# Performance work log

Hardware: AMD Instinct MI355X
Metric: run time of the kernel (lower is better)

## Reference

```python
import jax, jax.numpy as jnp
import numpy as np

USER_NUM = 100000
POI_NUM = 120
EMB = 64
HID1, HID2 = 256, 128
HEADS, ATT_H = 6, 8
SEQ = 5
CI_VOCAB = 50000
N_EDGES_U = 1600000


def _gcn_conv(x, edge_index, W, b, n):
    # PyG GCNConv: add self loops, symmetric D^-1/2 (A+I) D^-1/2 normalization
    x = x @ W
    loops = jnp.arange(n)
    src = jnp.concatenate([edge_index[0], loops])
    dst = jnp.concatenate([edge_index[1], loops])
    deg = jax.ops.segment_sum(jnp.ones_like(dst, x.dtype), dst, num_segments=n)
    dinv = jnp.where(deg > 0, jax.lax.rsqrt(deg), 0.0)
    norm = dinv[src] * dinv[dst]
    out = jax.ops.segment_sum(x[src] * norm[:, None], dst, num_segments=n)
    return out + b


def setup_inputs() -> dict:
    key = jax.random.key(0)
    ks = jax.random.split(key, 30)
    f = lambda k, shape, fan_in: (jax.random.normal(k, shape, jnp.float32) / np.sqrt(fan_in)).astype(jnp.float32)
    inp = {}
    inp['edge_user'] = jnp.stack([
        jax.random.randint(ks[0], (USER_NUM, SEQ), 0, USER_NUM),
        jax.random.randint(ks[1], (USER_NUM, SEQ), 0, CI_VOCAB)])
    inp['edge_poi'] = jax.random.randint(ks[2], (2, 4000), 0, POI_NUM)
    inp['u_v_edge'] = jax.random.randint(ks[3], (2, N_EDGES_U), 0, USER_NUM)
    inp['v_u_edge'] = jax.random.randint(ks[4], (2, 4000), 0, POI_NUM)
    inp['user_table'] = f(ks[5], (USER_NUM, EMB), EMB)
    inp['ci_table'] = f(ks[6], (CI_VOCAB, EMB), EMB)
    inp['ci_table2'] = f(ks[7], (CI_VOCAB, EMB), EMB)
    inp['gcn1_w'] = f(ks[8], (EMB, EMB), EMB)
    inp['gcn1_b'] = jnp.zeros((EMB,), jnp.float32)
    inp['gcn2_w'] = f(ks[9], (EMB, EMB), EMB)
    inp['gcn2_b'] = jnp.zeros((EMB,), jnp.float32)
    inp['at_w'] = f(ks[10], (HEADS, EMB, ATT_H), EMB)
    inp['at_b'] = jnp.zeros((HEADS, ATT_H), jnp.float32)
    inp['d2_w'] = f(ks[11], (1 + HEADS * ATT_H, 1), 1 + HEADS * ATT_H)  # Linear(49,1)
    inp['d2_b'] = jnp.zeros((1,), jnp.float32)
    inp['d1u_w'] = f(ks[12], (EMB, HID1), EMB)
    inp['d1u_b'] = jnp.zeros((HID1,), jnp.float32)
    inp['d2u_w'] = f(ks[13], (HID1, HID2), HID1)
    inp['d2u_b'] = jnp.zeros((HID2,), jnp.float32)
    inp['d3u_w'] = f(ks[14], (HID2, POI_NUM), HID2)
    inp['d3u_b'] = jnp.zeros((POI_NUM,), jnp.float32)
    inp['d1_w'] = f(ks[15], (EMB, POI_NUM), EMB)  # dense1_: Linear(n_emb, 120)
    inp['d1_b'] = jnp.zeros((POI_NUM,), jnp.float32)
    return inp


def reference(edge_user, edge_poi, u_v_edge, v_u_edge, user_table, ci_table, ci_table2,
              gcn1_w, gcn1_b, gcn2_w, gcn2_b, at_w, at_b, d2_w, d2_b,
              d1u_w, d1u_b, d2u_w, d2u_b, d3u_w, d3u_b, d1_w, d1_b):
    # user GCN stack (dropout treated as identity / eval mode)
    ue = _gcn_conv(user_table, u_v_edge, gcn1_w, gcn1_b, USER_NUM)
    ue = jax.nn.relu(ue)
    ue = _gcn_conv(ue, u_v_edge, gcn2_w, gcn2_b, USER_NUM)  # (U, EMB)

    ci_ids = edge_user[1]            # (U, SEQ) check-in ids
    ci = ci_table[ci_ids]            # (U, SEQ, EMB)
    ci2 = ci_table2[ci_ids]          # (U, SEQ, EMB)

    # batched multi-head tiny attention: softmax over the SEQ axis per user
    w = jnp.einsum('usd,hdk->uhsk', ci, at_w) + at_b[None, :, None, :]
    beta = jax.nn.softmax(jnp.tanh(w), axis=2)                       # (U, H, SEQ, ATT_H)
    beta = jnp.transpose(beta, (0, 2, 1, 3)).reshape(ci.shape[0], SEQ, HEADS * ATT_H)
    att = jnp.transpose(beta, (0, 2, 1))                              # (U, 48, SEQ)
    use_trans = att @ ci                                              # (U, 48, EMB)

    uef = jnp.concatenate([ue[:, None, :], use_trans], axis=1)       # (U, 49, EMB)
    uef = jnp.transpose(uef, (0, 2, 1)) @ d2_w + d2_b                # (U, EMB, 1)
    uef = uef[..., 0]                                                # (U, EMB)

    h = jax.nn.relu(uef @ d1u_w + d1u_b)
    h = jax.nn.relu(h @ d2u_w + d2u_b)
    score1 = h @ d3u_w + d3u_b                                       # (U, POI_NUM)

    score2 = jnp.sum(ci2 @ d1_w + d1_b, axis=1)                      # (U, POI_NUM)
    return score1 + score2
```

## Files before the change

### kernel.cpp

```cpp
#include <hip/hip_runtime.h>

#define U_NUM 100000
#define NE    1600000
#define SEQL  5

#define OFF_DEG      0UL
#define OFF_CURSOR   400000UL
#define OFF_ROWSTART 800000UL
#define OFF_DINV     1200016UL
#define OFF_BSUM     1600016UL
#define OFF_CSR      1600528UL
#define OFF_XS       8000528UL
#define OFF_B        20800528UL
#define OFF_CI2B     46400528UL
#define OFF_CIB      52800528UL

#define NB    196
#define BSH   9
#define BCAP  12240
#define OFF_BINS  OFF_XS
#define OFF_GCUR  (OFF_BINS + (size_t)NB * BCAP * 8)

typedef __attribute__((ext_vector_type(8))) short bf16x8;
typedef __attribute__((ext_vector_type(4))) float f32x4;

__device__ __forceinline__ float rd_lane(float v, int l) {
    return __int_as_float(__builtin_amdgcn_readlane(__float_as_int(v), l));
}

__device__ __forceinline__ short f2bf(float f) {
    unsigned u = __float_as_uint(f);
    unsigned r = (u + 0x7fffu + ((u >> 16) & 1u)) >> 16;
    return (short)r;
}

__device__ __forceinline__ unsigned pk2(float a, float b) {
    return ((unsigned)(unsigned short)f2bf(a)) | (((unsigned)(unsigned short)f2bf(b)) << 16);
}

__device__ __forceinline__ float bflo(unsigned p) { return __uint_as_float(p << 16); }
__device__ __forceinline__ float bfhi(unsigned p) { return __uint_as_float(p & 0xffff0000u); }

__device__ __forceinline__ int swzo(int row, int bytecol, int rowstride) {
    return row * rowstride + (bytecol ^ ((row & 7) << 4));
}

__global__ __launch_bounds__(256) void k_count(const int* __restrict__ edge, int* __restrict__ deg) {
    int e = blockIdx.x * 256 + threadIdx.x;
    atomicAdd(&deg[edge[NE + e]], 1);
}

__global__ __launch_bounds__(256) void k_dinv(const int* __restrict__ deg, float* __restrict__ dinv) {
    int i = blockIdx.x * 256 + threadIdx.x;
    if (i < U_NUM) dinv[i] = rsqrtf((float)(deg[i] + 1));
}

__global__ __launch_bounds__(256) void k_cvt2(const float* __restrict__ src, unsigned* __restrict__ dst) {
    int i = blockIdx.x * 256 + threadIdx.x;
    float2 v = *(const float2*)(src + (size_t)i * 2);
    dst[i] = pk2(v.x, v.y);
}

__global__ __launch_bounds__(1024) void k_scanA(const int* __restrict__ deg, int* __restrict__ bsum) {
    __shared__ int sm[1024];
    int i = blockIdx.x * 1024 + threadIdx.x;
    sm[threadIdx.x] = (i < U_NUM) ? deg[i] : 0;
    __syncthreads();
    for (int off = 512; off > 0; off >>= 1) {
        if (threadIdx.x < off) sm[threadIdx.x] += sm[threadIdx.x + off];
        __syncthreads();
    }
    if (threadIdx.x == 0) bsum[blockIdx.x] = sm[0];
}

__global__ void k_scanB(int* bsum, int nb) {
    if (threadIdx.x == 0) {
        int acc = 0;
        for (int b = 0; b < nb; ++b) { int v = bsum[b]; bsum[b] = acc; acc += v; }
    }
}

__global__ __launch_bounds__(1024) void k_scanC(const int* __restrict__ deg, const int* __restrict__ bsum,
                                                int* __restrict__ row_start) {
    __shared__ int sm[1024];
    int t = threadIdx.x;
    int i = blockIdx.x * 1024 + t;
    int v = (i < U_NUM) ? deg[i] : 0;
    sm[t] = v;
    __syncthreads();
    for (int off = 1; off < 1024; off <<= 1) {
        int x = (t >= off) ? sm[t - off] : 0;
        __syncthreads();
        sm[t] += x;
        __syncthreads();
    }
    int incl = sm[t];
    int base = bsum[blockIdx.x];
    if (i < U_NUM) row_start[i] = base + incl - v;
    if (i == U_NUM - 1) row_start[U_NUM] = base + incl;
}

__global__ __launch_bounds__(256) void k_binA(const int* __restrict__ edge,
                                              unsigned* __restrict__ gcur,
                                              uint2* __restrict__ bins) {
    __shared__ int hist[256];
    __shared__ int startx[256];
    __shared__ int cur[256];
    __shared__ int gbase[256];
    __shared__ uint2 stage[4096];
    int t = threadIdx.x;
    int base = blockIdx.x * 4096;
    hist[t] = 0; cur[t] = 0;
    __syncthreads();
    int src[16], dst[16];
#pragma unroll
    for (int j = 0; j < 16; ++j) {
        int e = base + j * 256 + t;
        src[j] = 0; dst[j] = -1;
        if (e < NE) {
            src[j] = edge[e];
            dst[j] = edge[NE + e];
            atomicAdd(&hist[dst[j] >> BSH], 1);
        }
    }
    __syncthreads();
    startx[t] = hist[t];
    __syncthreads();
    for (int off = 1; off < 256; off <<= 1) {
        int v = (t >= off) ? startx[t - off] : 0;
        __syncthreads();
        startx[t] += v;
        __syncthreads();
    }
    {
        int ex = startx[t] - hist[t];
        __syncthreads();
        startx[t] = ex;
    }
    if (t < NB) gbase[t] = (int)atomicAdd(&gcur[t], (unsigned)hist[t]);
    __syncthreads();
#pragma unroll
    for (int j = 0; j < 16; ++j) {
        if (dst[j] >= 0) {
            int b = dst[j] >> BSH;
            int p = startx[b] + atomicAdd(&cur[b], 1);
            stage[p] = make_uint2((unsigned)src[j], (unsigned)dst[j]);
        }
    }
    __syncthreads();
    int cnt = NE - base; if (cnt > 4096) cnt = 4096;
    for (int p = t; p < cnt; p += 256) {
        uint2 v = stage[p];
        int b = (int)(v.y >> BSH);
        bins[(size_t)b * BCAP + gbase[b] + (p - startx[b])] = v;
    }
}

__global__ __launch_bounds__(256) void k_fillB(const uint2* __restrict__ bins,
                                               const unsigned* __restrict__ gcur,
                                               const int* __restrict__ row_start,
                                               int* __restrict__ csr) {
    __shared__ int cur[512];
    int b = blockIdx.x, t = threadIdx.x;
    cur[t] = 0; cur[t + 256] = 0;
    __syncthreads();
    int cnt = (int)gcur[b];
    int d0 = b << BSH;
    for (int i = t; i < cnt; i += 256) {
        uint2 e = bins[(size_t)b * BCAP + i];
        int d = (int)e.y;
        int pos = row_start[d] + atomicAdd(&cur[d - d0], 1);
        csr[pos] = (int)e.x;
    }
}

__global__ __launch_bounds__(256) void k_gemm64_mfma(
        const float* __restrict__ x, const float* __restrict__ w,
        const float* __restrict__ dinv, unsigned* __restrict__ outb, int relu_in) {
    __shared__ __align__(16) short Xa[64 * 64];
    __shared__ float dv[64];
    int t = threadIdx.x;
    int lane = t & 63, wid = t >> 6;
    int l15 = lane & 15, lg = lane >> 4;
    bf16x8 wf[2];
#pragma unroll
    for (int ks = 0; ks < 2; ++ks) {
        int col = wid * 16 + l15;
        int kb = ks * 32 + lg * 8;
        bf16x8 f;
#pragma unroll
        for (int j = 0; j < 8; ++j) f[j] = f2bf(w[(kb + j) * 64 + col]);
        wf[ks] = f;
    }
    int u0 = blockIdx.x * 64;
    {
        int ur = t >> 2, d0 = (t & 3) * 16;
        int u = u0 + ur;
        float xv[16];
        if (u < U_NUM) {
            const float4* up = (const float4*)(x + (size_t)u * 64 + d0);
#pragma unroll
            for (int q = 0; q < 4; ++q) {
                float4 v = up[q];
                xv[q * 4 + 0] = v.x; xv[q * 4 + 1] = v.y; xv[q * 4 + 2] = v.z; xv[q * 4 + 3] = v.w;
            }
        } else {
#pragma unroll
            for (int q = 0; q < 16; ++q) xv[q] = 0.f;
        }
        if (relu_in) {
#pragma unroll
            for (int q = 0; q < 16; ++q) xv[q] = fmaxf(xv[q], 0.f);
        }
        bf16x8 p0, p1;
#pragma unroll
        for (int j = 0; j < 8; ++j) { p0[j] = f2bf(xv[j]); p1[j] = f2bf(xv[8 + j]); }
        *(bf16x8*)((char*)Xa + swzo(ur, d0 * 2, 128)) = p0;
        *(bf16x8*)((char*)Xa + swzo(ur, d0 * 2 + 16, 128)) = p1;
        if (t < 64) {
            int uu = u0 + t;
            dv[t] = dinv[(uu < U_NUM) ? uu : (U_NUM - 1)];
        }
    }
    __syncthreads();
#pragma unroll
    for (int mt = 0; mt < 4; ++mt) {
        bf16x8 a0 = *(bf16x8*)((char*)Xa + swzo(mt * 16 + l15, lg * 16, 128));
        bf16x8 a1 = *(bf16x8*)((char*)Xa + swzo(mt * 16 + l15, 64 + lg * 16, 128));
        f32x4 c = {0.f, 0.f, 0.f, 0.f};
        c = __builtin_amdgcn_mfma_f32_16x16x32_bf16(a0, wf[0], c, 0, 0, 0);
        c = __builtin_amdgcn_mfma_f32_16x16x32_bf16(a1, wf[1], c, 0, 0, 0);
        int col = wid * 16 + l15;
#pragma unroll
        for (int r = 0; r < 4; ++r) {
            int row = mt * 16 + lg * 4 + r;
            float v = c[r] * dv[row];
            float other = __shfl_xor(v, 1);
            int u = u0 + row;
            if (!(l15 & 1) && u < U_NUM)
                outb[(size_t)u * 32 + (col >> 1)] = pk2(v, other);
        }
    }
}

__global__ __launch_bounds__(256) void k_gather2(const unsigned* __restrict__ xs, const float* __restrict__ dinv,
                                                 const int* __restrict__ row_start, const int* __restrict__ csr,
                                                 const float* __restrict__ bias, float* __restrict__ outb) {
    int i = blockIdx.x * 4 + (threadIdx.x >> 6);
    int lane = threadIdx.x & 63, half = lane >> 5, sl = lane & 31;
    int s0 = row_start[i], s1 = row_start[i + 1];
    float di = dinv[i];
    float accx = 0.f, accy = 0.f;
    if (!half) {
        unsigned pk = xs[(size_t)i * 32 + sl];
        accx = bflo(pk); accy = bfhi(pk);
    }
    int e = s0 + half;
    for (; e + 14 < s1; e += 16) {
        int id0 = csr[e], id1 = csr[e + 2], id2 = csr[e + 4], id3 = csr[e + 6];
        int id4 = csr[e + 8], id5 = csr[e + 10], id6 = csr[e + 12], id7 = csr[e + 14];
        unsigned p0 = xs[(size_t)id0 * 32 + sl];
        unsigned p1 = xs[(size_t)id1 * 32 + sl];
        unsigned p2 = xs[(size_t)id2 * 32 + sl];
        unsigned p3 = xs[(size_t)id3 * 32 + sl];
        unsigned p4 = xs[(size_t)id4 * 32 + sl];
        unsigned p5 = xs[(size_t)id5 * 32 + sl];
        unsigned p6 = xs[(size_t)id6 * 32 + sl];
        unsigned p7 = xs[(size_t)id7 * 32 + sl];
        accx += ((bflo(p0) + bflo(p1)) + (bflo(p2) + bflo(p3))) +
                ((bflo(p4) + bflo(p5)) + (bflo(p6) + bflo(p7)));
        accy += ((bfhi(p0) + bfhi(p1)) + (bfhi(p2) + bfhi(p3))) +
                ((bfhi(p4) + bfhi(p5)) + (bfhi(p6) + bfhi(p7)));
    }
    for (; e < s1; e += 2) {
        unsigned pa = xs[(size_t)csr[e] * 32 + sl];
        accx += bflo(pa);
        accy += bfhi(pa);
    }
    accx += __shfl_xor(accx, 32);
    accy += __shfl_xor(accy, 32);
    if (!half) {
        float2 bb = *(const float2*)(bias + sl * 2);
        float2 o;
        o.x = fmaf(accx, di, bb.x);
        o.y = fmaf(accy, di, bb.y);
        *(float2*)(outb + (size_t)i * 64 + sl * 2) = o;
    }
}

#define AUB 32

__global__ __launch_bounds__(256) void k_attn_mfma(
        const int* __restrict__ edge_user, const unsigned* __restrict__ cib,
        const unsigned* __restrict__ ci2b,
        const float* __restrict__ at_w, const float* __restrict__ at_b,
        const float* __restrict__ d2_w, const float* __restrict__ d2_b,
        const float* ue, unsigned* uefc) {
    __shared__ __align__(16) short CI[256 * 64];
    int t = threadIdx.x;
    int lane = t & 63, wid = t >> 6;
    int l15 = lane & 15, lg = lane >> 4;
    int half = lane >> 5, sl = lane & 31;

    bf16x8 bw[3][2];
#pragma unroll
    for (int nt = 0; nt < 3; ++nt) {
        int j48 = nt * 16 + l15;
        int h = j48 >> 3, kk = j48 & 7;
#pragma unroll
        for (int ks = 0; ks < 2; ++ks) {
            int kb = ks * 32 + lg * 8;
            bf16x8 f;
#pragma unroll
            for (int j = 0; j < 8; ++j) f[j] = f2bf(at_w[h * 512 + (kb + j) * 8 + kk]);
            bw[nt][ks] = f;
        }
    }
    float atbv[3], dcoef[3];
#pragma unroll
    for (int nt = 0; nt < 3; ++nt) {
        atbv[nt] = at_b[nt * 16 + l15];
        dcoef[nt] = d2_w[1 + nt * 16 + l15];
    }
    float d2w0 = d2_w[0], d2b0 = d2_b[0];

    int u0 = blockIdx.x * AUB;
    float accx[8], accy[8];
#pragma unroll
    for (int j = 0; j < 8; ++j) { accx[j] = 0.f; accy[j] = 0.f; }
#pragma unroll
    for (int j = 0; j < 8; ++j) {
#pragma unroll
        for (int q = 0; q < 4; ++q) {
            int s = q * 2 + half;
            int row = wid * 64 + j * 8 + s;
            unsigned pk = 0;
            if (s < 5) {
                int id = edge_user[U_NUM * SEQL + (u0 + wid * 8 + j) * SEQL + s];
                pk = cib[(size_t)id * 32 + sl];
                unsigned pc = ci2b[(size_t)id * 32 + sl];
                accx[j] += bflo(pc);
                accy[j] += bfhi(pc);
            }
            *(unsigned*)((char*)CI + swzo(row, sl * 4, 128)) = pk;
        }
    }
    __syncthreads();

    float evenm = (lg & 1) ? 0.f : 1.f;
    for (int mt = 0; mt < 4; ++mt) {
        int tbase = (wid * 4 + mt) * 16;
        bf16x8 a0 = *(bf16x8*)((char*)CI + swzo(tbase + l15, lg * 16, 128));
        bf16x8 a1 = *(bf16x8*)((char*)CI + swzo(tbase + l15, 64 + lg * 16, 128));
        float g0 = 0.f, g1 = 0.f, g2 = 0.f, g3 = 0.f;
#pragma unroll
        for (int nt = 0; nt < 3; ++nt) {
            f32x4 c = {0.f, 0.f, 0.f, 0.f};
            c = __builtin_amdgcn_mfma_f32_16x16x32_bf16(a0, bw[nt][0], c, 0, 0, 0);
            c = __builtin_amdgcn_mfma_f32_16x16x32_bf16(a1, bw[nt][1], c, 0, 0, 0);
            float w0 = c[0] + atbv[nt], w1 = c[1] + atbv[nt],
                  w2 = c[2] + atbv[nt], w3 = c[3] + atbv[nt];
            float e0 = __expf(1.f - __fdividef(2.f, __expf(2.f * w0) + 1.f));
            float e1 = __expf(1.f - __fdividef(2.f, __expf(2.f * w1) + 1.f));
            float e2 = __expf(1.f - __fdividef(2.f, __expf(2.f * w2) + 1.f));
            float e3 = __expf(1.f - __fdividef(2.f, __expf(2.f * w3) + 1.f));
            float partial = e0 + evenm * (e1 + e2 + e3);
            float esum = partial + __shfl_xor(partial, 16);
            float sc = __fdividef(dcoef[nt], esum);
            g0 = fmaf(e0, sc, g0);
            g1 = fmaf(e1, sc, g1);
            g2 = fmaf(e2, sc, g2);
            g3 = fmaf(e3, sc, g3);
        }
#pragma unroll
        for (int d = 1; d < 16; d <<= 1) {
            g0 += __shfl_xor(g0, d);
            g1 += __shfl_xor(g1, d);
            g2 += __shfl_xor(g2, d);
            g3 += __shfl_xor(g3, d);
        }
        float gA0 = rd_lane(g0, 0), gA1 = rd_lane(g1, 0), gA2 = rd_lane(g2, 0),
              gA3 = rd_lane(g3, 0), gA4 = rd_lane(g0, 16);
        float gB0 = rd_lane(g0, 32), gB1 = rd_lane(g1, 32), gB2 = rd_lane(g2, 32),
              gB3 = rd_lane(g3, 32), gB4 = rd_lane(g0, 48);
        float gs0 = half ? gB0 : gA0;
        float gs1 = half ? gB1 : gA1;
        float gs2 = half ? gB2 : gA2;
        float gs3 = half ? gB3 : gA3;
        float gs4 = half ? gB4 : gA4;
        int urow = tbase + half * 8;
        int u = u0 + (tbase >> 3) + half;
        float2 uev = *(const float2*)(ue + (size_t)u * 64 + sl * 2);
        float rx = fmaf(d2w0, uev.x, d2b0);
        float ry = fmaf(d2w0, uev.y, d2b0);
        unsigned c0 = *(unsigned*)((char*)CI + swzo(urow + 0, sl * 4, 128));
        unsigned c1 = *(unsigned*)((char*)CI + swzo(urow + 1, sl * 4, 128));
        unsigned c2 = *(unsigned*)((char*)CI + swzo(urow + 2, sl * 4, 128));
        unsigned c3 = *(unsigned*)((char*)CI + swzo(urow + 3, sl * 4, 128));
        unsigned c4 = *(unsigned*)((char*)CI + swzo(urow + 4, sl * 4, 128));
        rx = fmaf(gs0, bflo(c0), rx); ry = fmaf(gs0, bfhi(c0), ry);
        rx = fmaf(gs1, bflo(c1), rx); ry = fmaf(gs1, bfhi(c1), ry);
        rx = fmaf(gs2, bflo(c2), rx); ry = fmaf(gs2, bfhi(c2), ry);
        rx = fmaf(gs3, bflo(c3), rx); ry = fmaf(gs3, bfhi(c3), ry);
        rx = fmaf(gs4, bflo(c4), rx); ry = fmaf(gs4, bfhi(c4), ry);
        uefc[(size_t)u * 64 + sl] = pk2(rx, ry);
    }
#pragma unroll
    for (int j = 0; j < 8; ++j) {
        float ax = accx[j] + __shfl_xor(accx[j], 32);
        float ay = accy[j] + __shfl_xor(accy[j], 32);
        if (!half) {
            int u = u0 + wid * 8 + j;
            uefc[(size_t)u * 64 + 32 + sl] = pk2(ax, ay);
        }
    }
}

#define N_TILES 1563

__global__ __launch_bounds__(512, 4) void k_mlp_mfma(
        const unsigned* __restrict__ uefc,
        const float* __restrict__ w1, const float* __restrict__ b1,
        const float* __restrict__ w2, const float* __restrict__ b2,
        const float* __restrict__ w3, const float* __restrict__ b3,
        const float* __restrict__ dw, const float* __restrict__ db,
        float* __restrict__ out) {
    __shared__ __align__(16) short Xa[64 * 64];
    __shared__ __align__(16) short Ca[64 * 64];
    __shared__ __align__(16) short h1a[64 * 256];
    __shared__ __align__(16) short h2c[64 * 128];
    int t = threadIdx.x;
    int lane = t & 63, w = t >> 6;
    int l15 = lane & 15, lg = lane >> 4;

    bf16x8 wf1[4];
#pragma unroll
    for (int nt = 0; nt < 2; ++nt)
#pragma unroll
        for (int ks = 0; ks < 2; ++ks) {
            int col = w * 32 + nt * 16 + l15;
            int kb = ks * 32 + lg * 8;
            bf16x8 f;
#pragma unroll
            for (int j = 0; j < 8; ++j) f[j] = f2bf(w1[(kb + j) * 256 + col]);
            wf1[nt * 2 + ks] = f;
        }
    bf16x8 wf2[8];
#pragma unroll
    for (int ks = 0; ks < 8; ++ks) {
        int col = w * 16 + l15;
        int kb = ks * 32 + lg * 8;
        bf16x8 f;
#pragma unroll
        for (int j = 0; j < 8; ++j) f[j] = f2bf(w2[(kb + j) * 128 + col]);
        wf2[ks] = f;
    }
    bf16x8 wf3[6];
#pragma unroll
    for (int ks = 0; ks < 6; ++ks) {
        int col = w * 16 + l15;
        int kb = ks * 32 + lg * 8;
        bf16x8 f;
#pragma unroll
        for (int j = 0; j < 8; ++j) {
            int k = kb + j;
            float v = 0.f;
            if (col < 120) v = (k < 128) ? w3[k * 120 + col] : dw[(k - 128) * 120 + col];
            f[j] = f2bf(v);
        }
        wf3[ks] = f;
    }
    float bias1[2], bias2, bias3;
#pragma unroll
    for (int nt = 0; nt < 2; ++nt) bias1[nt] = b1[w * 32 + nt * 16 + l15];
    {
        int col = w * 16 + l15;
        bias2 = b2[col];
        bias3 = (col < 120) ? (b3[col] + 5.f * db[col]) : 0.f;
    }

    int ur = t >> 3, q = t & 7;
    for (int tile = blockIdx.x; tile < N_TILES; tile += gridDim.x) {
        int u0 = tile * 64;
        {
            size_t u = (size_t)u0 + ur;
            uint4 A0 = {0, 0, 0, 0}, A1 = A0;
            if (u < U_NUM) {
                const uint4* up = (const uint4*)(uefc + u * 64 + q * 8);
                A0 = up[0]; A1 = up[1];
            }
            char* base = (q < 4) ? ((char*)Xa) : ((char*)Ca);
            int bc = (q & 3) * 32;
            *(uint4*)(base + swzo(ur, bc, 128)) = A0;
            *(uint4*)(base + swzo(ur, bc + 16, 128)) = A1;
        }
        __syncthreads();
#pragma unroll
        for (int mt = 0; mt < 4; ++mt) {
            bf16x8 a0 = *(bf16x8*)((char*)Xa + swzo(mt * 16 + l15, lg * 16, 128));
            bf16x8 a1 = *(bf16x8*)((char*)Xa + swzo(mt * 16 + l15, 64 + lg * 16, 128));
#pragma unroll
            for (int nt = 0; nt < 2; ++nt) {
                f32x4 c = {0.f, 0.f, 0.f, 0.f};
                c = __builtin_amdgcn_mfma_f32_16x16x32_bf16(a0, wf1[nt * 2 + 0], c, 0, 0, 0);
                c = __builtin_amdgcn_mfma_f32_16x16x32_bf16(a1, wf1[nt * 2 + 1], c, 0, 0, 0);
                int col = w * 32 + nt * 16 + l15;
                float bb = bias1[nt];
#pragma unroll
                for (int r = 0; r < 4; ++r) {
                    int row = mt * 16 + lg * 4 + r;
                    *(short*)((char*)h1a + swzo(row, col * 2, 512)) = f2bf(fmaxf(c[r] + bb, 0.f));
                }
            }
        }
        __syncthreads();
#pragma unroll
        for (int mt = 0; mt < 4; ++mt) {
            bf16x8 af[8];
#pragma unroll
            for (int ks = 0; ks < 8; ++ks)
                af[ks] = *(bf16x8*)((char*)h1a + swzo(mt * 16 + l15, ks * 64 + lg * 16, 512));
            f32x4 c = {0.f, 0.f, 0.f, 0.f};
#pragma unroll
            for (int ks = 0; ks < 8; ++ks)
                c = __builtin_amdgcn_mfma_f32_16x16x32_bf16(af[ks], wf2[ks], c, 0, 0, 0);
            int col = w * 16 + l15;
#pragma unroll
            for (int r = 0; r < 4; ++r) {
                int row = mt * 16 + lg * 4 + r;
                *(short*)((char*)h2c + swzo(row, col * 2, 256)) = f2bf(fmaxf(c[r] + bias2, 0.f));
            }
        }
        __syncthreads();
        float* Obuf = (float*)h1a;
#pragma unroll
        for (int mt = 0; mt < 4; ++mt) {
            bf16x8 af[6];
#pragma unroll
            for (int ks = 0; ks < 4; ++ks)
                af[ks] = *(bf16x8*)((char*)h2c + swzo(mt * 16 + l15, ks * 64 + lg * 16, 256));
#pragma unroll
            for (int ks = 4; ks < 6; ++ks)
                af[ks] = *(bf16x8*)((char*)Ca + swzo(mt * 16 + l15, (ks - 4) * 64 + lg * 16, 128));
            f32x4 c = {0.f, 0.f, 0.f, 0.f};
#pragma unroll
            for (int ks = 0; ks < 6; ++ks)
                c = __builtin_amdgcn_mfma_f32_16x16x32_bf16(af[ks], wf3[ks], c, 0, 0, 0);
            int col = w * 16 + l15;
            if (col < 120) {
#pragma unroll
                for (int r = 0; r < 4; ++r)
                    Obuf[(mt * 16 + lg * 4 + r) * 124 + col] = c[r] + bias3;
            }
        }
        __syncthreads();
        {
            int nrow = (U_NUM - u0 < 64) ? (U_NUM - u0) : 64;
            int nfl4 = nrow * 30;
            for (int i = t; i < nfl4; i += 512) {
                int row = i / 30, ch = i - row * 30;
                float4 v = *(const float4*)(Obuf + row * 124 + ch * 4);
                *(float4*)(out + (size_t)(u0 + row) * 120 + ch * 4) = v;
            }
        }
        __syncthreads();
    }
}

extern "C" void kernel_launch(void* const* d_in, const int* in_sizes, int n_in,
                              void* d_out, int out_size, void* d_ws, size_t ws_size,
                              hipStream_t stream) {
    const int* edge_user   = (const int*)d_in[0];
    const int* u_v_edge    = (const int*)d_in[2];
    const float* user_table = (const float*)d_in[4];
    const float* ci_table   = (const float*)d_in[5];
    const float* ci_table2  = (const float*)d_in[6];
    const float* gcn1_w = (const float*)d_in[7];
    const float* gcn1_b = (const float*)d_in[8];
    const float* gcn2_w = (const float*)d_in[9];
    const float* gcn2_b = (const float*)d_in[10];
    const float* at_w = (const float*)d_in[11];
    const float* at_b = (const float*)d_in[12];
    const float* d2_w = (const float*)d_in[13];
    const float* d2_b = (const float*)d_in[14];
    const float* d1u_w = (const float*)d_in[15];
    const float* d1u_b = (const float*)d_in[16];
    const float* d2u_w = (const float*)d_in[17];
    const float* d2u_b = (const float*)d_in[18];
    const float* d3u_w = (const float*)d_in[19];
    const float* d3u_b = (const float*)d_in[20];
    const float* d1_w = (const float*)d_in[21];
    const float* d1_b = (const float*)d_in[22];
    float* out = (float*)d_out;
    char* ws = (char*)d_ws;

    int* deg       = (int*)(ws + OFF_DEG);
    int* row_start = (int*)(ws + OFF_ROWSTART);
    float* dinv    = (float*)(ws + OFF_DINV);
    int* bsum      = (int*)(ws + OFF_BSUM);
    int* csr       = (int*)(ws + OFF_CSR);
    unsigned* XS   = (unsigned*)(ws + OFF_XS);
    float* B       = (float*)(ws + OFF_B);
    unsigned* CI2B = (unsigned*)(ws + OFF_CI2B);
    unsigned* CIB  = (unsigned*)(ws + OFF_CIB);
    uint2* bins    = (uint2*)(ws + OFF_BINS);
    unsigned* gcur = (unsigned*)(ws + OFF_GCUR);

    hipMemsetAsync(ws, 0, 400000, stream);
    hipMemsetAsync(ws + OFF_GCUR, 0, NB * 4, stream);
    k_count<<<6250, 256, 0, stream>>>(u_v_edge, deg);
    k_cvt2<<<6250, 256, 0, stream>>>(ci_table, CIB);
    k_cvt2<<<6250, 256, 0, stream>>>(ci_table2, CI2B);
    k_dinv<<<391, 256, 0, stream>>>(deg, dinv);
    k_scanA<<<98, 1024, 0, stream>>>(deg, bsum);
    k_scanB<<<1, 64, 0, stream>>>(bsum, 98);
    k_scanC<<<98, 1024, 0, stream>>>(deg, bsum, row_start);
    k_binA<<<391, 256, 0, stream>>>(u_v_edge, gcur, bins);
    k_fillB<<<NB, 256, 0, stream>>>(bins, gcur, row_start, csr);

    k_gemm64_mfma<<<1563, 256, 0, stream>>>(user_table, gcn1_w, dinv, XS, 0);
    k_gather2<<<25000, 256, 0, stream>>>(XS, dinv, row_start, csr, gcn1_b, B);
    k_gemm64_mfma<<<1563, 256, 0, stream>>>(B, gcn2_w, dinv, XS, 1);
    k_gather2<<<25000, 256, 0, stream>>>(XS, dinv, row_start, csr, gcn2_b, B);

    k_attn_mfma<<<3125, 256, 0, stream>>>(edge_user, CIB, CI2B, at_w, at_b, d2_w, d2_b,
                                          B, (unsigned*)B);
    k_mlp_mfma<<<512, 512, 0, stream>>>((const unsigned*)B,
                                        d1u_w, d1u_b, d2u_w, d2u_b, d3u_w, d3u_b, d1_w, d1_b, out);
}
```

Measured before the change: 469.6 us.

## Fuse attention stage into persistent MLP kernel via shared-memory handoff

Merges the attention kernel into the persistent MLP kernel. Each 64-user tile now gathers check-in embeddings, runs the attention MFMAs and writes the per-user feature and ci2 sum straight into the shared-memory MLP input buffers, so the uefc intermediate no longer makes a round trip through global memory and one launch is removed. Attention weights are staged once per block in LDS and the h1 buffer is reused as gather scratch. Output stores become nontemporal. In exchange, the grid drops to 512 persistent blocks, so fewer waves are in flight to hide the random embedding gathers, and LDS use per block grows, which may lower occupancy.

```diff
diff --git a/kernel.cpp b/kernel.cpp
--- a/kernel.cpp
+++ b/kernel.cpp
@@ -5,7 +5,6 @@
 #define SEQL  5
 
 #define OFF_DEG      0UL
-#define OFF_CURSOR   400000UL
 #define OFF_ROWSTART 800000UL
 #define OFF_DINV     1200016UL
 #define OFF_BSUM     1600016UL
@@ -288,150 +287,27 @@
     }
 }
 
-#define AUB 32
-
-__global__ __launch_bounds__(256) void k_attn_mfma(
+#define N_TILES 1563
+
+__global__ __launch_bounds__(512, 4) void k_attn_mlp(
         const int* __restrict__ edge_user, const unsigned* __restrict__ cib,
-        const unsigned* __restrict__ ci2b,
+        const unsigned* __restrict__ ci2b, const float* __restrict__ ue,
         const float* __restrict__ at_w, const float* __restrict__ at_b,
         const float* __restrict__ d2_w, const float* __restrict__ d2_b,
-        const float* ue, unsigned* uefc) {
-    __shared__ __align__(16) short CI[256 * 64];
-    int t = threadIdx.x;
-    int lane = t & 63, wid = t >> 6;
-    int l15 = lane & 15, lg = lane >> 4;
-    int half = lane >> 5, sl = lane & 31;
-
-    bf16x8 bw[3][2];
-#pragma unroll
-    for (int nt = 0; nt < 3; ++nt) {
-        int j48 = nt * 16 + l15;
-        int h = j48 >> 3, kk = j48 & 7;
-#pragma unroll
-        for (int ks = 0; ks < 2; ++ks) {
-            int kb = ks * 32 + lg * 8;
-            bf16x8 f;
-#pragma unroll
-            for (int j = 0; j < 8; ++j) f[j] = f2bf(at_w[h * 512 + (kb + j) * 8 + kk]);
-            bw[nt][ks] = f;
-        }
-    }
-    float atbv[3], dcoef[3];
-#pragma unroll
-    for (int nt = 0; nt < 3; ++nt) {
-        atbv[nt] = at_b[nt * 16 + l15];
-        dcoef[nt] = d2_w[1 + nt * 16 + l15];
-    }
-    float d2w0 = d2_w[0], d2b0 = d2_b[0];
-
-    int u0 = blockIdx.x * AUB;
-    float accx[8], accy[8];
-#pragma unroll
-    for (int j = 0; j < 8; ++j) { accx[j] = 0.f; accy[j] = 0.f; }
-#pragma unroll
-    for (int j = 0; j < 8; ++j) {
-#pragma unroll
-        for (int q = 0; q < 4; ++q) {
-            int s = q * 2 + half;
-            int row = wid * 64 + j * 8 + s;
-            unsigned pk = 0;
-            if (s < 5) {
-                int id = edge_user[U_NUM * SEQL + (u0 + wid * 8 + j) * SEQL + s];
-                pk = cib[(size_t)id * 32 + sl];
-                unsigned pc = ci2b[(size_t)id * 32 + sl];
-                accx[j] += bflo(pc);
-                accy[j] += bfhi(pc);
-            }
-            *(unsigned*)((char*)CI + swzo(row, sl * 4, 128)) = pk;
-        }
-    }
-    __syncthreads();
-
-    float evenm = (lg & 1) ? 0.f : 1.f;
-    for (int mt = 0; mt < 4; ++mt) {
-        int tbase = (wid * 4 + mt) * 16;
-        bf16x8 a0 = *(bf16x8*)((char*)CI + swzo(tbase + l15, lg * 16, 128));
-        bf16x8 a1 = *(bf16x8*)((char*)CI + swzo(tbase + l15, 64 + lg * 16, 128));
-        float g0 = 0.f, g1 = 0.f, g2 = 0.f, g3 = 0.f;
-#pragma unroll
-        for (int nt = 0; nt < 3; ++nt) {
-            f32x4 c = {0.f, 0.f, 0.f, 0.f};
-            c = __builtin_amdgcn_mfma_f32_16x16x32_bf16(a0, bw[nt][0], c, 0, 0, 0);
-            c = __builtin_amdgcn_mfma_f32_16x16x32_bf16(a1, bw[nt][1], c, 0, 0, 0);
-            float w0 = c[0] + atbv[nt], w1 = c[1] + atbv[nt],
-                  w2 = c[2] + atbv[nt], w3 = c[3] + atbv[nt];
-            float e0 = __expf(1.f - __fdividef(2.f, __expf(2.f * w0) + 1.f));
-            float e1 = __expf(1.f - __fdividef(2.f, __expf(2.f * w1) + 1.f));
-            float e2 = __expf(1.f - __fdividef(2.f, __expf(2.f * w2) + 1.f));
-            float e3 = __expf(1.f - __fdividef(2.f, __expf(2.f * w3) + 1.f));
-            float partial = e0 + evenm * (e1 + e2 + e3);
-            float esum = partial + __shfl_xor(partial, 16);
-            float sc = __fdividef(dcoef[nt], esum);
-            g0 = fmaf(e0, sc, g0);
-            g1 = fmaf(e1, sc, g1);
-            g2 = fmaf(e2, sc, g2);
-            g3 = fmaf(e3, sc, g3);
-        }
-#pragma unroll
-        for (int d = 1; d < 16; d <<= 1) {
-            g0 += __shfl_xor(g0, d);
-            g1 += __shfl_xor(g1, d);
-            g2 += __shfl_xor(g2, d);
-            g3 += __shfl_xor(g3, d);
-        }
-        float gA0 = rd_lane(g0, 0), gA1 = rd_lane(g1, 0), gA2 = rd_lane(g2, 0),
-              gA3 = rd_lane(g3, 0), gA4 = rd_lane(g0, 16);
-        float gB0 = rd_lane(g0, 32), gB1 = rd_lane(g1, 32), gB2 = rd_lane(g2, 32),
-              gB3 = rd_lane(g3, 32), gB4 = rd_lane(g0, 48);
-        float gs0 = half ? gB0 : gA0;
-        float gs1 = half ? gB1 : gA1;
-        float gs2 = half ? gB2 : gA2;
-        float gs3 = half ? gB3 : gA3;
-        float gs4 = half ? gB4 : gA4;
-        int urow = tbase + half * 8;
-        int u = u0 + (tbase >> 3) + half;
-        float2 uev = *(const float2*)(ue + (size_t)u * 64 + sl * 2);
-        float rx = fmaf(d2w0, uev.x, d2b0);
-        float ry = fmaf(d2w0, uev.y, d2b0);
-        unsigned c0 = *(unsigned*)((char*)CI + swzo(urow + 0, sl * 4, 128));
-        unsigned c1 = *(unsigned*)((char*)CI + swzo(urow + 1, sl * 4, 128));
-        unsigned c2 = *(unsigned*)((char*)CI + swzo(urow + 2, sl * 4, 128));
-        unsigned c3 = *(unsigned*)((char*)CI + swzo(urow + 3, sl * 4, 128));
-        unsigned c4 = *(unsigned*)((char*)CI + swzo(urow + 4, sl * 4, 128));
-        rx = fmaf(gs0, bflo(c0), rx); ry = fmaf(gs0, bfhi(c0), ry);
-        rx = fmaf(gs1, bflo(c1), rx); ry = fmaf(gs1, bfhi(c1), ry);
-        rx = fmaf(gs2, bflo(c2), rx); ry = fmaf(gs2, bfhi(c2), ry);
-        rx = fmaf(gs3, bflo(c3), rx); ry = fmaf(gs3, bfhi(c3), ry);
-        rx = fmaf(gs4, bflo(c4), rx); ry = fmaf(gs4, bfhi(c4), ry);
-        uefc[(size_t)u * 64 + sl] = pk2(rx, ry);
-    }
-#pragma unroll
-    for (int j = 0; j < 8; ++j) {
-        float ax = accx[j] + __shfl_xor(accx[j], 32);
-        float ay = accy[j] + __shfl_xor(accy[j], 32);
-        if (!half) {
-            int u = u0 + wid * 8 + j;
-            uefc[(size_t)u * 64 + 32 + sl] = pk2(ax, ay);
-        }
-    }
-}
-
-#define N_TILES 1563
-
-__global__ __launch_bounds__(512, 4) void k_mlp_mfma(
-        const unsigned* __restrict__ uefc,
         const float* __restrict__ w1, const float* __restrict__ b1,
         const float* __restrict__ w2, const float* __restrict__ b2,
         const float* __restrict__ w3, const float* __restrict__ b3,
         const float* __restrict__ dw, const float* __restrict__ db,
         float* __restrict__ out) {
+    __shared__ __align__(16) short hbuf[64 * 256];
     __shared__ __align__(16) short Xa[64 * 64];
     __shared__ __align__(16) short Ca[64 * 64];
-    __shared__ __align__(16) short h1a[64 * 256];
     __shared__ __align__(16) short h2c[64 * 128];
+    __shared__ __align__(16) short BWL[6 * 64 * 8];
     int t = threadIdx.x;
     int lane = t & 63, w = t >> 6;
     int l15 = lane & 15, lg = lane >> 4;
+    int half = lane >> 5, sl = lane & 31;
 
     bf16x8 wf1[4];
 #pragma unroll
@@ -478,21 +354,123 @@
         bias2 = b2[col];
         bias3 = (col < 120) ? (b3[col] + 5.f * db[col]) : 0.f;
     }
-
-    int ur = t >> 3, q = t & 7;
+    float atbv[3], dcoef[3];
+#pragma unroll
+    for (int nt = 0; nt < 3; ++nt) {
+        atbv[nt] = at_b[nt * 16 + l15];
+        dcoef[nt] = d2_w[1 + nt * 16 + l15];
+    }
+    float d2w0 = d2_w[0], d2b0 = d2_b[0];
+    if (t < 64) {
+#pragma unroll
+        for (int nt = 0; nt < 3; ++nt) {
+            int j48 = nt * 16 + l15;
+            int hh = j48 >> 3, kk = j48 & 7;
+#pragma unroll
+            for (int ks = 0; ks < 2; ++ks) {
+                int kb = ks * 32 + lg * 8;
+                bf16x8 f;
+#pragma unroll
+                for (int j = 0; j < 8; ++j) f[j] = f2bf(at_w[hh * 512 + (kb + j) * 8 + kk]);
+                *(bf16x8*)(BWL + ((nt * 2 + ks) * 64 + lane) * 8) = f;
+            }
+        }
+    }
+    __syncthreads();
+
+    float evenm = (lg & 1) ? 0.f : 1.f;
     for (int tile = blockIdx.x; tile < N_TILES; tile += gridDim.x) {
         int u0 = tile * 64;
-        {
-            size_t u = (size_t)u0 + ur;
-            uint4 A0 = {0, 0, 0, 0}, A1 = A0;
-            if (u < U_NUM) {
-                const uint4* up = (const uint4*)(uefc + u * 64 + q * 8);
-                A0 = up[0]; A1 = up[1];
-            }
-            char* base = (q < 4) ? ((char*)Xa) : ((char*)Ca);
-            int bc = (q & 3) * 32;
-            *(uint4*)(base + swzo(ur, bc, 128)) = A0;
-            *(uint4*)(base + swzo(ur, bc + 16, 128)) = A1;
+#pragma unroll
+        for (int hh = 0; hh < 2; ++hh) {
+            float accx[4] = {0.f, 0.f, 0.f, 0.f}, accy[4] = {0.f, 0.f, 0.f, 0.f};
+#pragma unroll
+            for (int j = 0; j < 4; ++j) {
+#pragma unroll
+                for (int q = 0; q < 4; ++q) {
+                    int s = q * 2 + half;
+                    int row = w * 32 + j * 8 + s;
+                    int uu = u0 + 32 * hh + w * 4 + j;
+                    unsigned pk = 0;
+                    if (s < 5 && uu < U_NUM) {
+                        int id = edge_user[U_NUM * SEQL + uu * SEQL + s];
+                        pk = cib[(size_t)id * 32 + sl];
+                        unsigned pc = ci2b[(size_t)id * 32 + sl];
+                        accx[j] += bflo(pc);
+                        accy[j] += bfhi(pc);
+                    }
+                    *(unsigned*)((char*)hbuf + swzo(row, sl * 4, 128)) = pk;
+                }
+            }
+#pragma unroll
+            for (int mt = 0; mt < 2; ++mt) {
+                int tbase = w * 32 + mt * 16;
+                bf16x8 a0 = *(bf16x8*)((char*)hbuf + swzo(tbase + l15, lg * 16, 128));
+                bf16x8 a1 = *(bf16x8*)((char*)hbuf + swzo(tbase + l15, 64 + lg * 16, 128));
+                float g0 = 0.f, g1 = 0.f, g2 = 0.f, g3 = 0.f;
+#pragma unroll
+                for (int nt = 0; nt < 3; ++nt) {
+                    bf16x8 b0 = *(const bf16x8*)(BWL + ((nt * 2 + 0) * 64 + lane) * 8);
+                    bf16x8 b1f = *(const bf16x8*)(BWL + ((nt * 2 + 1) * 64 + lane) * 8);
+                    f32x4 c = {0.f, 0.f, 0.f, 0.f};
+                    c = __builtin_amdgcn_mfma_f32_16x16x32_bf16(a0, b0, c, 0, 0, 0);
+                    c = __builtin_amdgcn_mfma_f32_16x16x32_bf16(a1, b1f, c, 0, 0, 0);
+                    float w0 = c[0] + atbv[nt], w1v = c[1] + atbv[nt],
+                          w2v = c[2] + atbv[nt], w3v = c[3] + atbv[nt];
+                    float e0 = __expf(1.f - __fdividef(2.f, __expf(2.f * w0) + 1.f));
+                    float e1 = __expf(1.f - __fdividef(2.f, __expf(2.f * w1v) + 1.f));
+                    float e2 = __expf(1.f - __fdividef(2.f, __expf(2.f * w2v) + 1.f));
+                    float e3 = __expf(1.f - __fdividef(2.f, __expf(2.f * w3v) + 1.f));
+                    float partial = e0 + evenm * (e1 + e2 + e3);
+                    float esum = partial + __shfl_xor(partial, 16);
+                    float sc = __fdividef(dcoef[nt], esum);
+                    g0 = fmaf(e0, sc, g0);
+                    g1 = fmaf(e1, sc, g1);
+                    g2 = fmaf(e2, sc, g2);
+                    g3 = fmaf(e3, sc, g3);
+                }
+#pragma unroll
+                for (int d = 1; d < 16; d <<= 1) {
+                    g0 += __shfl_xor(g0, d);
+                    g1 += __shfl_xor(g1, d);
+                    g2 += __shfl_xor(g2, d);
+                    g3 += __shfl_xor(g3, d);
+                }
+                float gA0 = rd_lane(g0, 0), gA1 = rd_lane(g1, 0), gA2 = rd_lane(g2, 0),
+                      gA3 = rd_lane(g3, 0), gA4 = rd_lane(g0, 16);
+                float gB0 = rd_lane(g0, 32), gB1 = rd_lane(g1, 32), gB2 = rd_lane(g2, 32),
+                      gB3 = rd_lane(g3, 32), gB4 = rd_lane(g0, 48);
+                float gs0 = half ? gB0 : gA0;
+                float gs1 = half ? gB1 : gA1;
+                float gs2 = half ? gB2 : gA2;
+                float gs3 = half ? gB3 : gA3;
+                float gs4 = half ? gB4 : gA4;
+                int urow = tbase + half * 8;
+                int ul = 32 * hh + w * 4 + mt * 2 + half;
+                int u = u0 + ul;
+                float2 uev = make_float2(0.f, 0.f);
+                if (u < U_NUM) uev = *(const float2*)(ue + (size_t)u * 64 + sl * 2);
+                float rx = fmaf(d2w0, uev.x, d2b0);
+                float ry = fmaf(d2w0, uev.y, d2b0);
+                unsigned c0 = *(unsigned*)((char*)hbuf + swzo(urow + 0, sl * 4, 128));
+                unsigned c1 = *(unsigned*)((char*)hbuf + swzo(urow + 1, sl * 4, 128));
+                unsigned c2 = *(unsigned*)((char*)hbuf + swzo(urow + 2, sl * 4, 128));
+                unsigned c3 = *(unsigned*)((char*)hbuf + swzo(urow + 3, sl * 4, 128));
+                unsigned c4 = *(unsigned*)((char*)hbuf + swzo(urow + 4, sl * 4, 128));
+                rx = fmaf(gs0, bflo(c0), rx); ry = fmaf(gs0, bfhi(c0), ry);
+                rx = fmaf(gs1, bflo(c1), rx); ry = fmaf(gs1, bfhi(c1), ry);
+                rx = fmaf(gs2, bflo(c2), rx); ry = fmaf(gs2, bfhi(c2), ry);
+                rx = fmaf(gs3, bflo(c3), rx); ry = fmaf(gs3, bfhi(c3), ry);
+                rx = fmaf(gs4, bflo(c4), rx); ry = fmaf(gs4, bfhi(c4), ry);
+                *(unsigned*)((char*)Xa + swzo(ul, sl * 4, 128)) = pk2(rx, ry);
+            }
+#pragma unroll
+            for (int j = 0; j < 4; ++j) {
+                float ax = accx[j] + __shfl_xor(accx[j], 32);
+                float ay = accy[j] + __shfl_xor(accy[j], 32);
+                if (!half)
+                    *(unsigned*)((char*)Ca + swzo(32 * hh + w * 4 + j, sl * 4, 128)) = pk2(ax, ay);
+            }
         }
         __syncthreads();
 #pragma unroll
@@ -509,7 +487,7 @@
 #pragma unroll
                 for (int r = 0; r < 4; ++r) {
                     int row = mt * 16 + lg * 4 + r;
-                    *(short*)((char*)h1a + swzo(row, col * 2, 512)) = f2bf(fmaxf(c[r] + bb, 0.f));
+                    *(short*)((char*)hbuf + swzo(row, col * 2, 512)) = f2bf(fmaxf(c[r] + bb, 0.f));
                 }
             }
         }
@@ -519,7 +497,7 @@
             bf16x8 af[8];
 #pragma unroll
             for (int ks = 0; ks < 8; ++ks)
-                af[ks] = *(bf16x8*)((char*)h1a + swzo(mt * 16 + l15, ks * 64 + lg * 16, 512));
+                af[ks] = *(bf16x8*)((char*)hbuf + swzo(mt * 16 + l15, ks * 64 + lg * 16, 512));
             f32x4 c = {0.f, 0.f, 0.f, 0.f};
 #pragma unroll
             for (int ks = 0; ks < 8; ++ks)
@@ -532,7 +510,7 @@
             }
         }
         __syncthreads();
-        float* Obuf = (float*)h1a;
+        float* Obuf = (float*)hbuf;
 #pragma unroll
         for (int mt = 0; mt < 4; ++mt) {
             bf16x8 af[6];
@@ -559,8 +537,8 @@
             int nfl4 = nrow * 30;
             for (int i = t; i < nfl4; i += 512) {
                 int row = i / 30, ch = i - row * 30;
-                float4 v = *(const float4*)(Obuf + row * 124 + ch * 4);
-                *(float4*)(out + (size_t)(u0 + row) * 120 + ch * 4) = v;
+                f32x4 v = *(const f32x4*)(Obuf + row * 124 + ch * 4);
+                __builtin_nontemporal_store(v, (f32x4*)(out + (size_t)(u0 + row) * 120 + ch * 4));
             }
         }
         __syncthreads();
@@ -606,8 +584,8 @@
     uint2* bins    = (uint2*)(ws + OFF_BINS);
     unsigned* gcur = (unsigned*)(ws + OFF_GCUR);
 
-    hipMemsetAsync(ws, 0, 400000, stream);
-    hipMemsetAsync(ws + OFF_GCUR, 0, NB * 4, stream);
+    (void)hipMemsetAsync(ws, 0, 400000, stream);
+    (void)hipMemsetAsync(ws + OFF_GCUR, 0, NB * 4, stream);
     k_count<<<6250, 256, 0, stream>>>(u_v_edge, deg);
     k_cvt2<<<6250, 256, 0, stream>>>(ci_table, CIB);
     k_cvt2<<<6250, 256, 0, stream>>>(ci_table2, CI2B);
@@ -623,8 +601,7 @@
     k_gemm64_mfma<<<1563, 256, 0, stream>>>(B, gcn2_w, dinv, XS, 1);
     k_gather2<<<25000, 256, 0, stream>>>(XS, dinv, row_start, csr, gcn2_b, B);
 
-    k_attn_mfma<<<3125, 256, 0, stream>>>(edge_user, CIB, CI2B, at_w, at_b, d2_w, d2_b,
-                                          B, (unsigned*)B);
-    k_mlp_mfma<<<512, 512, 0, stream>>>((const unsigned*)B,
+    k_attn_mlp<<<512, 512, 0, stream>>>(edge_user, CIB, CI2B, B,
+                                        at_w, at_b, d2_w, d2_b,
                                         d1u_w, d1u_b, d2u_w, d2u_b, d3u_w, d3u_b, d1_w, d1_b, out);
 }
```

Result: slower. 591.6 us (+26.0%).
